# Kernel tuning notes

Hardware: AMD Instinct MI355X
Metric: run time of the kernel (lower is better)

The kernel has to match this reference:

```python
import jax, jax.numpy as jnp
import numpy as np

N_TRANSFORMS = 24
N_INIT = 5
SOFT_BLEND = 5.0
MAX_STEPS = 8   # reduced from 50 for reference runtime; same per-step math
CVG = 1e-5
DVG = 1.0
EPS = 1e-6


def posi_enc(x):
    # min_deg=0, max_deg=4, append_identity: [...,3] -> [...,27]
    scales = jnp.asarray([1.0, 2.0, 4.0, 8.0], x.dtype)
    xb = (x[..., None, :] * scales[:, None]).reshape(x.shape[:-1] + (12,))
    return jnp.concatenate([x, jnp.sin(xb), jnp.cos(xb)], axis=-1)


def mlp(h, params):
    for W, b in params[:-1]:
        h = jax.nn.relu(h @ W + b)
    W, b = params[-1]
    return h @ W + b


def setup_inputs() -> dict:
    key = jax.random.key(0)
    ks = jax.random.split(key, 16)
    B, N, J = 1, 32768, N_TRANSFORMS
    x = jax.random.normal(ks[0], (B, N, 3), jnp.float32)
    bone_pts = jax.random.normal(ks[1], (J, 3), jnp.float32)

    def near_id(k):
        A = jnp.eye(4, dtype=jnp.float32) + 0.05 * jax.random.normal(k, (J, 4, 4), jnp.float32)
        return A.at[:, 3, :].set(jnp.asarray([0.0, 0.0, 0.0, 1.0], jnp.float32))

    inp = dict(
        x=x, bone_pts=bone_pts,
        transforms=near_id(ks[2]), delta_transforms=near_id(ks[3]),
        W0=0.1 * jax.random.normal(ks[4], (27, 128), jnp.float32), b0=jnp.zeros((128,), jnp.float32),
        W1=0.1 * jax.random.normal(ks[5], (128, 128), jnp.float32), b1=jnp.zeros((128,), jnp.float32),
        W2=0.1 * jax.random.normal(ks[6], (128, 128), jnp.float32), b2=jnp.zeros((128,), jnp.float32),
        W3=0.1 * jax.random.normal(ks[7], (128, 128), jnp.float32), b3=jnp.zeros((128,), jnp.float32),
        W4=0.1 * jax.random.normal(ks[8], (128, 25), jnp.float32), b4=jnp.zeros((25,), jnp.float32),
    )
    return inp


def reference(x, bone_pts, transforms, delta_transforms, W0, b0, W1, b1, W2, b2, W3, b3, W4, b4):
    params = [(W0, b0), (W1, b1), (W2, b2), (W3, b3), (W4, b4)]
    B, N, _ = x.shape
    I = N_INIT + 1  # with_bkgd appends identity init
    dt = x.dtype

    # ---- _initialize_canonical: KNN over bone distances, gather delta transforms
    d = jnp.linalg.norm(x[:, :, None, :] - bone_pts, axis=-1)          # [B,N,J]
    idx = jax.lax.top_k(-d, N_INIT)[1]                                  # [B,N,5]
    Tsel = delta_transforms[idx]                                        # [B,N,5,4,4]
    eye4 = jnp.broadcast_to(jnp.eye(4, dtype=dt), (B, N, 1, 4, 4))
    Tinit = jnp.concatenate([Tsel, eye4], axis=2)                       # [B,N,I,4,4]
    xh = jnp.concatenate([x, jnp.ones_like(x[..., :1])], axis=-1)
    xc0 = jnp.einsum('bnipq,bnq->bnip', Tinit[..., :3, :4], xh)         # [B,N,I,3]

    M = B * N * I
    target = jnp.broadcast_to(x[:, :, None, :], (B, N, I, 3)).reshape(M, 3)
    x0 = xc0.reshape(M, 3)
    Tfull = jnp.concatenate([transforms, jnp.eye(4, dtype=dt)[None]], axis=0)  # [J+1,4,4]

    def g(xc):  # forward-skinning residual g(x_cano) = LBS(x_cano) - x_world
        w = jax.nn.softmax(SOFT_BLEND * mlp(posi_enc(xc), params), axis=-1)   # [M,25]
        tf = jnp.einsum('mj,jpq->mpq', w, Tfull)                               # [M,4,4]
        return jnp.einsum('mpq,mq->mp', tf[:, :3, :3], xc) + tf[:, :3, 3] - target

    # ---- Broyden with dense per-point masking (replaces torch boolean indexing)
    Jinv0 = jnp.broadcast_to(jnp.eye(3, dtype=dt), (M, 3, 3))
    gx0 = g(x0)
    upd0 = -(Jinv0 @ gx0[:, :, None])[:, :, 0]
    norm0 = jnp.linalg.norm(gx0, axis=-1)
    zeros3 = jnp.zeros((M, 3), dt)
    state = (x0, gx0, Jinv0, upd0, x0, norm0, zeros3, zeros3, jnp.ones((M,), bool))

    def body(_, s):
        xk, gx, Jinv, upd, xopt, nopt, dx, dgx, mask = s
        m3 = mask[:, None]
        dx = jnp.where(m3, upd, dx)
        xk = jnp.where(m3, xk + dx, xk)
        gnew = g(xk)
        dgx = jnp.where(m3, gnew - gx, dgx)
        gx = jnp.where(m3, gx + dgx, gx)
        gn = jnp.linalg.norm(gx, axis=-1)
        better = gn < nopt
        nopt = jnp.where(better, gn, nopt)
        xopt = jnp.where(better[:, None], xk, xopt)
        mask = (nopt > CVG) & (gn < DVG)
        vT = dx[:, None, :] @ Jinv                                      # [M,1,3]
        a = dx[:, :, None] - Jinv @ dgx[:, :, None]                      # [M,3,1]
        b = vT @ dgx[:, :, None]                                         # [M,1,1]
        b = b + jnp.where(b >= 0, EPS, -EPS)
        Jinv = jnp.where(mask[:, None, None], Jinv + (a / b) @ vT, Jinv)
        upd = jnp.where(m3, -(Jinv @ gx[:, :, None])[:, :, 0], upd)
        return (xk, gx, Jinv, upd, xopt, nopt, dx, dgx, mask)

    state = jax.lax.fori_loop(0, MAX_STEPS, body, state)
    xopt, nopt = state[4], state[5]
    xopt = jax.lax.stop_gradient(xopt)  # torch detaches the root solve
    valid = nopt < CVG

    # differentiable final forward skinning at the found canonical points
    w = jax.nn.softmax(SOFT_BLEND * mlp(posi_enc(xopt), params), axis=-1)
    tf = jnp.einsum('mj,jpq->mpq', w, Tfull)
    xw = jnp.einsum('mpq,mq->mp', tf[:, :3, :3], xopt) + tf[:, :3, 3]

    return (xw.reshape(B, N, I, 3), xopt.reshape(B, N, I, 3),
            nopt.reshape(B, N, I), valid.reshape(B, N, I))
```

## Files before the change

### kernel.cpp

```cpp
#include <hip/hip_runtime.h>
#include <math.h>

#define BLOCK 256
#define PPB 64
#define HP 132
#define WCOLS 2136
#define NTILES 56

typedef float v2f __attribute__((ext_vector_type(2)));

__device__ __forceinline__ v2f mkv2(float a, float b) {
    v2f r; r.x = a; r.y = b; return r;
}
__device__ __forceinline__ v2f pkfma(v2f a, v2f b, v2f c) {
#if __has_builtin(__builtin_elementwise_fma)
    return __builtin_elementwise_fma(a, b, c);
#else
    return mkv2(fmaf(a.x, b.x, c.x), fmaf(a.y, b.y, c.y));
#endif
}
__device__ __forceinline__ float f4el(const float4& v, int r) {
    return (r == 0) ? v.x : (r == 1) ? v.y : (r == 2) ? v.z : v.w;
}
__device__ __forceinline__ int col_base(int p) { return p * HP + ((p >> 2) << 3); }

__global__ void prep_kernel(const float* __restrict__ W0, const float* __restrict__ W1,
                            const float* __restrict__ W2, const float* __restrict__ W3,
                            const float* __restrict__ W4, const float* __restrict__ b4,
                            float* __restrict__ Wt, float* __restrict__ b4p) {
    const int d = blockIdx.x * blockDim.x + threadIdx.x;
    if (d < NTILES * 1024) {
        const int t = d >> 10, w = d & 1023;
        float v;
        if (t < 52) {
            const int r = w >> 7, rem = w & 127;
            const int half = rem >> 6, q = (rem >> 2) & 15, jl = rem & 3;
            const int col = q * 8 + half * 4 + jl;
            if (t < 4)       { const int k = t * 8 + r;        v = (k < 27) ? W0[k * 128 + col] : 0.f; }
            else if (t < 20) { const int k = (t - 4) * 8 + r;  v = W1[k * 128 + col]; }
            else if (t < 36) { const int k = (t - 20) * 8 + r; v = W2[k * 128 + col]; }
            else             { const int k = (t - 36) * 8 + r; v = W3[k * 128 + col]; }
        } else {
            const int r = w >> 5, rem = w & 31;
            const int half = (rem >> 4) & 1, s = (rem >> 2) & 3, jl = rem & 3;
            const int col = s * 8 + half * 4 + jl;
            const int k = (t - 52) * 32 + r;
            v = (col < 25) ? W4[k * 25 + col] : 0.f;
        }
        Wt[d] = v;
    }
    if (d < 32) b4p[d] = (d < 25) ? b4[d] : 0.f;
}

__device__ __forceinline__ void batch4(const float* wt, int r0, int cg,
                                       const float* hg, int k0,
                                       v2f* __restrict__ acc) {
    float4 h4[4];
#pragma unroll
    for (int p = 0; p < 4; ++p) h4[p] = *(const float4*)(hg + p * HP + k0);
    float4 w0[4], w1[4];
#pragma unroll
    for (int r = 0; r < 4; ++r) {
        w0[r] = *(const float4*)(wt + (r0 + r) * 128 + cg * 4);
        w1[r] = *(const float4*)(wt + (r0 + r) * 128 + 64 + cg * 4);
    }
#pragma unroll
    for (int r = 0; r < 4; ++r) {
        const v2f wa = mkv2(w0[r].x, w0[r].y), wb2 = mkv2(w0[r].z, w0[r].w);
        const v2f wc = mkv2(w1[r].x, w1[r].y), wd = mkv2(w1[r].z, w1[r].w);
#pragma unroll
        for (int p = 0; p < 4; ++p) {
            const float hv = f4el(h4[p], r);
            const v2f hh = mkv2(hv, hv);
            acc[p * 4 + 0] = pkfma(hh, wa, acc[p * 4 + 0]);
            acc[p * 4 + 1] = pkfma(hh, wb2, acc[p * 4 + 1]);
            acc[p * 4 + 2] = pkfma(hh, wc, acc[p * 4 + 2]);
            acc[p * 4 + 3] = pkfma(hh, wd, acc[p * 4 + 3]);
        }
    }
}

__global__ __launch_bounds__(BLOCK)
__attribute__((amdgpu_num_vgpr(128))) void snarf_kernel(
    const float* __restrict__ xin, const float* __restrict__ bone_pts,
    const float* __restrict__ transforms, const float* __restrict__ delta_tf,
    const float* __restrict__ Wt, const float* __restrict__ b0,
    const float* __restrict__ b1, const float* __restrict__ b2,
    const float* __restrict__ b3, const float* __restrict__ b4p,
    float* __restrict__ out, int Npts) {
    __shared__ float hL[4 * WCOLS];
    __shared__ float stL[25 * PPB];
    __shared__ float wb[2][1024];
    __shared__ int flags[4];
    const int tid = threadIdx.x;
    const int wid = tid >> 6;
    const int lane = tid & 63;
    const int p16 = lane & 15;
    const int sq = lane >> 4;
    const int cg = lane >> 2;
    const int gg = lane & 3;
    const int M = Npts * 6;
    const int m = blockIdx.x * PPB + wid * 16 + p16;
    const int mc = (m < M) ? m : (M - 1);
    const int n = mc / 6;
    const int i = mc - n * 6;

    float* hWv = &hL[wid * WCOLS];
    const float* hg = hWv + gg * 536;
    float* hwr = hWv + gg * 536 + 8 * cg;
    float* hq = hWv + col_base(p16);
    volatile float* st = &stL[wid * 16 + p16];
#define STS(idx) st[(idx) * PPB]

    const float tx = xin[n * 3 + 0], ty = xin[n * 3 + 1], tz = xin[n * 3 + 2];

    float xk0, xk1, xk2;
    if (i < 5) {
        float dprev = -1.0f;
        int jprev = -1;
        for (int r = 0; r <= i; ++r) {
            float bd = 3.4028235e38f;
            int bj = 0;
            for (int j = 0; j < 24; ++j) {
                const float ax = tx - bone_pts[j * 3 + 0];
                const float ay = ty - bone_pts[j * 3 + 1];
                const float az = tz - bone_pts[j * 3 + 2];
                const float d = sqrtf(ax * ax + ay * ay + az * az);
                const bool taken = (d < dprev) || (d == dprev && j <= jprev);
                if (!taken && d < bd) { bd = d; bj = j; }
            }
            dprev = bd;
            jprev = bj;
        }
        const float* T = delta_tf + jprev * 16;
        xk0 = fmaf(T[0], tx, fmaf(T[1], ty, fmaf(T[2], tz, T[3])));
        xk1 = fmaf(T[4], tx, fmaf(T[5], ty, fmaf(T[6], tz, T[7])));
        xk2 = fmaf(T[8], tx, fmaf(T[9], ty, fmaf(T[10], tz, T[11])));
    } else {
        xk0 = tx; xk1 = ty; xk2 = tz;
    }

    float gx0 = 0.f, gx1 = 0.f, gx2 = 0.f;
    bool mask = (m < M);

    int cur = 0;
    *(float4*)(&wb[0][0] + tid * 4) = *(const float4*)(Wt + tid * 4);
    __syncthreads();

    for (int step = -1; step < 8; ++step) {
        bool m3 = mask;
        if (step >= 0) {
            __syncthreads();
            if ((flags[0] | flags[1] | flags[2] | flags[3]) == 0) break;
            if (m3) {
                const float u0 = STS(9), u1 = STS(10), u2 = STS(11);
                STS(12) = u0; STS(13) = u1; STS(14) = u2;
                xk0 += u0; xk1 += u1; xk2 += u2;
            }
        }
        const float cx0 = xk0, cx1 = xk1, cx2 = xk2;

        {
            const float f = (float)(1 << sq);
            float sx, cxv, sy, cyv, sz, czv;
            sincosf(f * cx0, &sx, &cxv);
            sincosf(f * cx1, &sy, &cyv);
            sincosf(f * cx2, &sz, &czv);
            if (sq == 0) { hq[0] = cx0; hq[1] = cx1; hq[2] = cx2; }
            const int sb = 3 + sq * 3;
            hq[sb + 0] = sx;  hq[sb + 1] = sy;  hq[sb + 2] = sz;
            hq[sb + 12] = cxv; hq[sb + 13] = cyv; hq[sb + 14] = czv;
            if (sq == 3) {
                hq[27] = 0.f; hq[28] = 0.f; hq[29] = 0.f; hq[30] = 0.f; hq[31] = 0.f;
            }
        }

        __builtin_amdgcn_s_setprio(1);
#pragma unroll 1
        for (int L = 0; L < 4; ++L) {
            const int tbase = (L == 0) ? 0 : (4 + (L - 1) * 16);
            const int NT = (L == 0) ? 4 : 16;
            const float* bc = ((L == 0) ? b0 : (L == 1) ? b1 : (L == 2) ? b2 : b3) + 8 * cg;
            v2f acc[16];
            {
                const float4 b0v = *(const float4*)(bc);
                const float4 b1v = *(const float4*)(bc + 4);
#pragma unroll
                for (int p = 0; p < 4; ++p) {
                    acc[p * 4 + 0] = mkv2(b0v.x, b0v.y);
                    acc[p * 4 + 1] = mkv2(b0v.z, b0v.w);
                    acc[p * 4 + 2] = mkv2(b1v.x, b1v.y);
                    acc[p * 4 + 3] = mkv2(b1v.z, b1v.w);
                }
            }
#pragma unroll 1
            for (int t = 0; t < NT; ++t) {
                const float4 stg = *(const float4*)(Wt + (tbase + t + 1) * 1024 + tid * 4);
                batch4(&wb[cur][0], 0, cg, hg, t * 8, acc);
                batch4(&wb[cur][0], 4, cg, hg, t * 8 + 4, acc);
                *(float4*)(&wb[cur ^ 1][0] + tid * 4) = stg;
                __syncthreads();
                cur ^= 1;
            }
#pragma unroll
            for (int p = 0; p < 4; ++p) {
                float4 o0, o1;
                o0.x = fmaxf(acc[p * 4 + 0].x, 0.f); o0.y = fmaxf(acc[p * 4 + 0].y, 0.f);
                o0.z = fmaxf(acc[p * 4 + 1].x, 0.f); o0.w = fmaxf(acc[p * 4 + 1].y, 0.f);
                o1.x = fmaxf(acc[p * 4 + 2].x, 0.f); o1.y = fmaxf(acc[p * 4 + 2].y, 0.f);
                o1.z = fmaxf(acc[p * 4 + 3].x, 0.f); o1.w = fmaxf(acc[p * 4 + 3].y, 0.f);
                *(float4*)(hwr + p * HP) = o0;
                *(float4*)(hwr + p * HP + 4) = o1;
            }
        }

        {
            v2f la[4];
            const float4 bb0 = *(const float4*)(b4p + 8 * sq);
            const float4 bb1 = *(const float4*)(b4p + 8 * sq + 4);
            la[0] = mkv2(bb0.x, bb0.y); la[1] = mkv2(bb0.z, bb0.w);
            la[2] = mkv2(bb1.x, bb1.y); la[3] = mkv2(bb1.z, bb1.w);
#pragma unroll 1
            for (int t = 0; t < 4; ++t) {
                const int nt = (t < 3) ? (53 + t) : 0;
                const float4 stg = *(const float4*)(Wt + nt * 1024 + tid * 4);
                const float* wt = &wb[cur][0];
#pragma unroll 2
                for (int kb = 0; kb < 8; ++kb) {
                    const float4 h4 = *(const float4*)(hq + t * 32 + kb * 4);
#pragma unroll
                    for (int r = 0; r < 4; ++r) {
                        const float4 w0 = *(const float4*)(wt + (kb * 4 + r) * 32 + sq * 4);
                        const float4 w1 = *(const float4*)(wt + (kb * 4 + r) * 32 + 16 + sq * 4);
                        const float hv = f4el(h4, r);
                        const v2f hh = mkv2(hv, hv);
                        la[0] = pkfma(hh, mkv2(w0.x, w0.y), la[0]);
                        la[1] = pkfma(hh, mkv2(w0.z, w0.w), la[1]);
                        la[2] = pkfma(hh, mkv2(w1.x, w1.y), la[2]);
                        la[3] = pkfma(hh, mkv2(w1.z, w1.w), la[3]);
                    }
                }
                *(float4*)(&wb[cur ^ 1][0] + tid * 4) = stg;
                __syncthreads();
                cur ^= 1;
            }
            __builtin_amdgcn_s_setprio(0);
            float4 o0, o1;
            o0.x = la[0].x; o0.y = la[0].y; o0.z = la[1].x; o0.w = la[1].y;
            o1.x = la[2].x; o1.y = la[2].y; o1.z = la[3].x; o1.w = la[3].y;
            *(float4*)(hq + 8 * sq) = o0;
            *(float4*)(hq + 8 * sq + 4) = o1;
        }

        float l25[25];
        {
            const float4 r0 = *(const float4*)(hq + 0);
            const float4 r1 = *(const float4*)(hq + 4);
            const float4 r2 = *(const float4*)(hq + 8);
            const float4 r3 = *(const float4*)(hq + 12);
            const float4 r4 = *(const float4*)(hq + 16);
            const float4 r5 = *(const float4*)(hq + 20);
            l25[0] = r0.x; l25[1] = r0.y; l25[2] = r0.z; l25[3] = r0.w;
            l25[4] = r1.x; l25[5] = r1.y; l25[6] = r1.z; l25[7] = r1.w;
            l25[8] = r2.x; l25[9] = r2.y; l25[10] = r2.z; l25[11] = r2.w;
            l25[12] = r3.x; l25[13] = r3.y; l25[14] = r3.z; l25[15] = r3.w;
            l25[16] = r4.x; l25[17] = r4.y; l25[18] = r4.z; l25[19] = r4.w;
            l25[20] = r5.x; l25[21] = r5.y; l25[22] = r5.z; l25[23] = r5.w;
            l25[24] = hq[24];
        }

        float zm = -3.4028235e38f;
#pragma unroll
        for (int j = 0; j < 25; ++j) {
            l25[j] = 5.0f * l25[j];
            zm = fmaxf(zm, l25[j]);
        }
        float ssum = 0.f;
#pragma unroll
        for (int j = 0; j < 25; ++j) {
            l25[j] = expf(l25[j] - zm);
            ssum += l25[j];
        }
        const float inv = 1.0f / ssum;

        float tf[12];
#pragma unroll
        for (int r = 0; r < 12; ++r) tf[r] = 0.f;
#pragma unroll
        for (int j = 0; j < 24; ++j) {
            const float wj = l25[j] * inv;
            const float* T = transforms + j * 16;
#pragma unroll
            for (int r = 0; r < 12; ++r) tf[r] = fmaf(wj, T[r], tf[r]);
        }
        {
            const float wj = l25[24] * inv;
            tf[0] += wj; tf[5] += wj; tf[10] += wj;
        }
        const float r0 = fmaf(tf[0], cx0, fmaf(tf[1], cx1, fmaf(tf[2], cx2, tf[3])));
        const float r1 = fmaf(tf[4], cx0, fmaf(tf[5], cx1, fmaf(tf[6], cx2, tf[7])));
        const float r2 = fmaf(tf[8], cx0, fmaf(tf[9], cx1, fmaf(tf[10], cx2, tf[11])));

        const float g0 = r0 - tx, g1 = r1 - ty, g2 = r2 - tz;

        if (step == -1) {
            gx0 = g0; gx1 = g1; gx2 = g2;
            const float gn = sqrtf(g0 * g0 + g1 * g1 + g2 * g2);
            STS(21) = gn;
            STS(9) = -g0; STS(10) = -g1; STS(11) = -g2;
            STS(18) = xk0; STS(19) = xk1; STS(20) = xk2;
            STS(22) = r0; STS(23) = r1; STS(24) = r2;
            STS(12) = 0.f; STS(13) = 0.f; STS(14) = 0.f;
            STS(15) = 0.f; STS(16) = 0.f; STS(17) = 0.f;
            STS(0) = 1.f; STS(1) = 0.f; STS(2) = 0.f;
            STS(3) = 0.f; STS(4) = 1.f; STS(5) = 0.f;
            STS(6) = 0.f; STS(7) = 0.f; STS(8) = 1.f;
        } else {
            float J00 = STS(0), J01 = STS(1), J02 = STS(2);
            float J10 = STS(3), J11 = STS(4), J12 = STS(5);
            float J20 = STS(6), J21 = STS(7), J22 = STS(8);
            const float dx0 = STS(12), dx1 = STS(13), dx2 = STS(14);
            float dg0 = STS(15), dg1 = STS(16), dg2 = STS(17);
            float nopt = STS(21);
            if (m3) {
                dg0 = g0 - gx0; dg1 = g1 - gx1; dg2 = g2 - gx2;
                gx0 += dg0; gx1 += dg1; gx2 += dg2;
                STS(15) = dg0; STS(16) = dg1; STS(17) = dg2;
            }
            const float gn = sqrtf(gx0 * gx0 + gx1 * gx1 + gx2 * gx2);
            const bool better = gn < nopt;
            if (better) {
                nopt = gn;
                STS(21) = gn;
                STS(18) = xk0; STS(19) = xk1; STS(20) = xk2;
                STS(22) = r0; STS(23) = r1; STS(24) = r2;
            }
            mask = (nopt > 1e-5f) && (gn < 1.0f) && (m < M);

            const float v0 = dx0 * J00 + dx1 * J10 + dx2 * J20;
            const float v1 = dx0 * J01 + dx1 * J11 + dx2 * J21;
            const float v2 = dx0 * J02 + dx1 * J12 + dx2 * J22;
            const float Jd0 = J00 * dg0 + J01 * dg1 + J02 * dg2;
            const float Jd1 = J10 * dg0 + J11 * dg1 + J12 * dg2;
            const float Jd2 = J20 * dg0 + J21 * dg1 + J22 * dg2;
            const float a0 = dx0 - Jd0, a1 = dx1 - Jd1, a2 = dx2 - Jd2;
            float bden = v0 * dg0 + v1 * dg1 + v2 * dg2;
            bden += (bden >= 0.f) ? 1e-6f : -1e-6f;
            if (mask) {
                const float q0 = a0 / bden, q1 = a1 / bden, q2 = a2 / bden;
                J00 = fmaf(q0, v0, J00); J01 = fmaf(q0, v1, J01); J02 = fmaf(q0, v2, J02);
                J10 = fmaf(q1, v0, J10); J11 = fmaf(q1, v1, J11); J12 = fmaf(q1, v2, J12);
                J20 = fmaf(q2, v0, J20); J21 = fmaf(q2, v1, J21); J22 = fmaf(q2, v2, J22);
                STS(0) = J00; STS(1) = J01; STS(2) = J02;
                STS(3) = J10; STS(4) = J11; STS(5) = J12;
                STS(6) = J20; STS(7) = J21; STS(8) = J22;
            }
            if (m3) {
                STS(9) = -(J00 * gx0 + J01 * gx1 + J02 * gx2);
                STS(10) = -(J10 * gx0 + J11 * gx1 + J12 * gx2);
                STS(11) = -(J20 * gx0 + J21 * gx1 + J22 * gx2);
            }
        }
        {
            const unsigned long long b = __ballot(mask);
            if (lane == 0) flags[wid] = (b != 0ull) ? 1 : 0;
        }
    }

    if (sq == 0 && m < M) {
        const float nopt = STS(21);
        out[(size_t)m * 3 + 0] = STS(22);
        out[(size_t)m * 3 + 1] = STS(23);
        out[(size_t)m * 3 + 2] = STS(24);
        float* xopt_out = out + (size_t)M * 3;
        xopt_out[(size_t)m * 3 + 0] = STS(18);
        xopt_out[(size_t)m * 3 + 1] = STS(19);
        xopt_out[(size_t)m * 3 + 2] = STS(20);
        out[(size_t)M * 6 + m] = nopt;
        out[(size_t)M * 7 + m] = (nopt < 1e-5f) ? 1.0f : 0.0f;
    }
#undef STS
}

extern "C" void kernel_launch(void* const* d_in, const int* in_sizes, int n_in,
                              void* d_out, int out_size, void* d_ws, size_t ws_size,
                              hipStream_t stream) {
    const float* x = (const float*)d_in[0];
    const float* bone_pts = (const float*)d_in[1];
    const float* transforms = (const float*)d_in[2];
    const float* delta_tf = (const float*)d_in[3];
    const float* W0 = (const float*)d_in[4];
    const float* b0 = (const float*)d_in[5];
    const float* W1 = (const float*)d_in[6];
    const float* b1 = (const float*)d_in[7];
    const float* W2 = (const float*)d_in[8];
    const float* b2 = (const float*)d_in[9];
    const float* W3 = (const float*)d_in[10];
    const float* b3 = (const float*)d_in[11];
    const float* W4 = (const float*)d_in[12];
    const float* b4 = (const float*)d_in[13];
    float* out = (float*)d_out;

    float* Wt = (float*)d_ws;
    float* b4p = Wt + NTILES * 1024;

    prep_kernel<<<(NTILES * 1024 + 255) / 256, 256, 0, stream>>>(
        W0, W1, W2, W3, W4, b4, Wt, b4p);

    const int Npts = in_sizes[0] / 3;
    const int M = Npts * 6;
    const int blocks = (M + PPB - 1) / PPB;
    snarf_kernel<<<blocks, BLOCK, 0, stream>>>(
        x, bone_pts, transforms, delta_tf, Wt, b0, b1, b2, b3, b4p, out, Npts);
}
```

Before: 1.747 ms.

## Use fast intrinsics, split blend rows across quad lanes, stagger LDS stores

Result: slower. 2.797 ms (+60.1%).

```diff
diff --git a/kernel.cpp b/kernel.cpp
--- a/kernel.cpp
+++ b/kernel.cpp
@@ -1,5 +1,6 @@
 #include <hip/hip_runtime.h>
 #include <math.h>
+#include <stdint.h>
 
 #define BLOCK 256
 #define PPB 64
@@ -163,9 +164,9 @@
         {
             const float f = (float)(1 << sq);
             float sx, cxv, sy, cyv, sz, czv;
-            sincosf(f * cx0, &sx, &cxv);
-            sincosf(f * cx1, &sy, &cyv);
-            sincosf(f * cx2, &sz, &czv);
+            __sincosf(f * cx0, &sx, &cxv);
+            __sincosf(f * cx1, &sy, &cyv);
+            __sincosf(f * cx2, &sz, &czv);
             if (sq == 0) { hq[0] = cx0; hq[1] = cx1; hq[2] = cx2; }
             const int sb = 3 + sq * 3;
             hq[sb + 0] = sx;  hq[sb + 1] = sy;  hq[sb + 2] = sz;
@@ -176,9 +177,9 @@
         }
 
         __builtin_amdgcn_s_setprio(1);
+        int gt = 0;
 #pragma unroll 1
         for (int L = 0; L < 4; ++L) {
-            const int tbase = (L == 0) ? 0 : (4 + (L - 1) * 16);
             const int NT = (L == 0) ? 4 : 16;
             const float* bc = ((L == 0) ? b0 : (L == 1) ? b1 : (L == 2) ? b2 : b3) + 8 * cg;
             v2f acc[16];
@@ -195,15 +196,17 @@
             }
 #pragma unroll 1
             for (int t = 0; t < NT; ++t) {
-                const float4 stg = *(const float4*)(Wt + (tbase + t + 1) * 1024 + tid * 4);
+                const float4 stg = *(const float4*)(Wt + (gt + 1) * 1024 + tid * 4);
                 batch4(&wb[cur][0], 0, cg, hg, t * 8, acc);
                 batch4(&wb[cur][0], 4, cg, hg, t * 8 + 4, acc);
                 *(float4*)(&wb[cur ^ 1][0] + tid * 4) = stg;
                 __syncthreads();
                 cur ^= 1;
-            }
-#pragma unroll
-            for (int p = 0; p < 4; ++p) {
+                ++gt;
+            }
+#pragma unroll
+            for (int q = 0; q < 4; ++q) {
+                const int p = (q + (cg & 3)) & 3;
                 float4 o0, o1;
                 o0.x = fmaxf(acc[p * 4 + 0].x, 0.f); o0.y = fmaxf(acc[p * 4 + 0].y, 0.f);
                 o0.z = fmaxf(acc[p * 4 + 1].x, 0.f); o0.w = fmaxf(acc[p * 4 + 1].y, 0.f);
@@ -278,28 +281,38 @@
         float ssum = 0.f;
 #pragma unroll
         for (int j = 0; j < 25; ++j) {
-            l25[j] = expf(l25[j] - zm);
+            l25[j] = __expf(l25[j] - zm);
             ssum += l25[j];
         }
         const float inv = 1.0f / ssum;
 
-        float tf[12];
-#pragma unroll
-        for (int r = 0; r < 12; ++r) tf[r] = 0.f;
-#pragma unroll
-        for (int j = 0; j < 24; ++j) {
-            const float wj = l25[j] * inv;
-            const float* T = transforms + j * 16;
-#pragma unroll
-            for (int r = 0; r < 12; ++r) tf[r] = fmaf(wj, T[r], tf[r]);
-        }
+        float r0, r1, r2;
         {
-            const float wj = l25[24] * inv;
-            tf[0] += wj; tf[5] += wj; tf[10] += wj;
-        }
-        const float r0 = fmaf(tf[0], cx0, fmaf(tf[1], cx1, fmaf(tf[2], cx2, tf[3])));
-        const float r1 = fmaf(tf[4], cx0, fmaf(tf[5], cx1, fmaf(tf[6], cx2, tf[7])));
-        const float r2 = fmaf(tf[8], cx0, fmaf(tf[9], cx1, fmaf(tf[10], cx2, tf[11])));
+            const int rs = (sq < 3) ? sq : 0;
+            float tfr0 = 0.f, tfr1 = 0.f, tfr2 = 0.f, tfr3 = 0.f;
+#pragma unroll
+            for (int j = 0; j < 24; ++j) {
+                const float wj = l25[j] * inv;
+                const float* T = transforms + j * 16 + rs * 4;
+                tfr0 = fmaf(wj, T[0], tfr0);
+                tfr1 = fmaf(wj, T[1], tfr1);
+                tfr2 = fmaf(wj, T[2], tfr2);
+                tfr3 = fmaf(wj, T[3], tfr3);
+            }
+            {
+                const float wj = l25[24] * inv;
+                if (rs == 0) tfr0 += wj;
+                else if (rs == 1) tfr1 += wj;
+                else tfr2 += wj;
+            }
+            const float rr = fmaf(tfr0, cx0, fmaf(tfr1, cx1, fmaf(tfr2, cx2, tfr3)));
+            if (sq < 3) hq[29 + sq] = rr;
+            asm volatile("s_waitcnt lgkmcnt(0)" ::: "memory");
+            __builtin_amdgcn_sched_barrier(0);
+            r0 = hq[29]; r1 = hq[30]; r2 = hq[31];
+            asm volatile("s_waitcnt lgkmcnt(0)" ::: "memory");
+            __builtin_amdgcn_sched_barrier(0);
+        }
 
         const float g0 = r0 - tx, g1 = r1 - ty, g2 = r2 - tz;
 
```
